# Kernel tuning notes

Measured on AMD Instinct MI355X. Metric: run time of the kernel, lower is better.

The kernel has to match this reference:

```python
import jax, jax.numpy as jnp
import numpy as np

DECAY = 0.999
EPS = 1e-06
NUM_CLUSTERS = 512
NUM_HEADS = 8
DIM_PER_HEAD = 64


def setup_inputs() -> dict:
    key = jax.random.key(0)
    k1, k2 = jax.random.split(key)
    x = jax.random.normal(k1, (8, 2048, NUM_HEADS * DIM_PER_HEAD), dtype=jnp.float32)
    means = jax.random.normal(k2, (NUM_HEADS, NUM_CLUSTERS, DIM_PER_HEAD), dtype=jnp.float32)
    return {"x": x, "means": means}


def reference(x, means):
    b, n, _ = x.shape
    h, k, d = means.shape
    xh = x.reshape(b, n, h, d)  # 'b n (h d) -> b n h d'
    dists = (
        jnp.sum(xh ** 2, axis=-1)[..., None]
        - 2.0 * jnp.einsum('bnhd,hkd->bnhk', xh, means)
        + jnp.sum(means ** 2, axis=-1)[None, None, :, :]
    )
    cluster_ids = jnp.argmin(dists, axis=-1)  # [b, n, h] int
    # training-path EMA codebook update
    one_hot = jax.nn.one_hot(cluster_ids, k, dtype=jnp.float32)  # [b, n, h, k]
    per_cluster_count = jnp.sum(one_hot, axis=(0, 1))  # [h, k]
    sum_x = jnp.einsum('bnhk,bnhd->hkd', one_hot, xh)  # [h, k, d]
    new_means = sum_x / (EPS + per_cluster_count[..., None])
    updated_means = (1.0 - DECAY) * new_means + DECAY * means
    return cluster_ids, updated_means
```

## Files before the change

kernel.cpp:

```cpp
#include <hip/hip_runtime.h>

#define NUM_HEADS 8
#define DIM 64
#define NCLUST 512
#define NTOK 16384
#define ROWLEN 512
#define NIDS (NTOK * NUM_HEADS)
#define NMEANS (NUM_HEADS * NCLUST * DIM)
#define NCK (NUM_HEADS * NCLUST)
#define TPB 64
#define KQ 128
#define CAP 8
#define DELTA 0.35f

typedef unsigned long long u64;
typedef short bf16x8 __attribute__((ext_vector_type(8)));
typedef float f32x4 __attribute__((ext_vector_type(4)));

__device__ __forceinline__ unsigned short f2bf(float f) {
    unsigned b = __float_as_uint(f);
    return (unsigned short)((b + 0x7fffu + ((b >> 16) & 1u)) >> 16);
}
__device__ __forceinline__ unsigned pack2bf(float lo, float hi) {
    return (unsigned)f2bf(lo) | ((unsigned)f2bf(hi) << 16);
}
__device__ __forceinline__ float bf2f(unsigned short b) {
    return __uint_as_float((unsigned)b << 16);
}
__device__ __forceinline__ u64 packkey(float s, int k) {
    unsigned u = __float_as_uint(s);
    unsigned ord = (u & 0x80000000u) ? ~u : (u | 0x80000000u);
    return ((u64)(~ord) << 32) | (unsigned)k;
}
__device__ __forceinline__ int swz(int row, int byte_in_row) {
    return row * 128 + (byte_in_row ^ ((row & 7) << 4));
}

__global__ void vq_prep(const float* __restrict__ means,
                        float* __restrict__ q,
                        unsigned short* __restrict__ mbf) {
    int g = blockIdx.x * blockDim.x + threadIdx.x;
    int row = g >> 4, c = g & 15;
    float4 v = *(const float4*)(means + (size_t)row * DIM + c * 4);
    ushort4 b;
    b.x = f2bf(v.x); b.y = f2bf(v.y); b.z = f2bf(v.z); b.w = f2bf(v.w);
    *(ushort4*)(mbf + (size_t)row * DIM + c * 4) = b;
    float s = fmaf(v.x, v.x, fmaf(v.y, v.y, fmaf(v.z, v.z, v.w * v.w)));
#pragma unroll
    for (int off = 1; off < 16; off <<= 1) s += __shfl_xor(s, off, 64);
    if (c == 0) q[row] = 0.5f * s;
}

__global__ __launch_bounds__(256, 8) void vq_score(const float* __restrict__ x,
                                                   const float* __restrict__ means,
                                                   const unsigned short* __restrict__ mbf,
                                                   const float* __restrict__ q,
                                                   float* __restrict__ ids_f) {
    __shared__ __align__(16) unsigned char msq[KQ * 128];
    __shared__ float qs[NCLUST];
    __shared__ int cnt[TPB];
    __shared__ unsigned short candL[TPB][CAP];

    const int head = blockIdx.y;
    const int t0   = blockIdx.x * TPB;
    const int tid  = threadIdx.x;
    const int wv = tid >> 6, l = tid & 63;
    const int lg = l >> 4, lc = l & 15;
    const int twave = wv * 16;

    auto stage_async = [&](int qt) {
        const unsigned char* gbase = (const unsigned char*)mbf
            + ((size_t)head * NCLUST + (size_t)qt * KQ) * (DIM * 2);
        const int rloc = l >> 3;
        const int srcb = ((l & 7) << 4) ^ (rloc << 4);
#pragma unroll
        for (int i = 0; i < 4; ++i) {
            int chunk = wv * 4 + i;
            const unsigned char* src = gbase + (chunk * 8 + rloc) * 128 + srcb;
            __builtin_amdgcn_global_load_lds(
                (const __attribute__((address_space(1))) unsigned int*)src,
                (__attribute__((address_space(3))) unsigned int*)(msq + chunk * 1024),
                16, 0, 0);
        }
    };

    bf16x8 af[2];
    {
        const float* xrow = x + (size_t)(t0 + twave + lc) * ROWLEN + head * DIM;
#pragma unroll
        for (int ks = 0; ks < 2; ++ks) {
            float av[8];
            *(float4*)&av[0] = *(const float4*)(xrow + ks * 32 + lg * 8);
            *(float4*)&av[4] = *(const float4*)(xrow + ks * 32 + lg * 8 + 4);
#pragma unroll
            for (int j = 0; j < 8; ++j) af[ks][j] = (short)f2bf(av[j]);
        }
    }
    qs[tid] = q[head * NCLUST + tid];
    qs[tid + 256] = q[head * NCLUST + tid + 256];
    if (tid < TPB) cnt[tid] = 0;
    stage_async(0);
    __syncthreads();

    float best[4];
#pragma unroll
    for (int r = 0; r < 4; ++r) best[r] = -3.0e38f;
    float thr[4];

    auto sweep1_q = [&](int qt) {
        const int rbase = 511 - qt * KQ - lc;
#pragma unroll
        for (int ct = 0; ct < KQ / 16; ++ct) {
            bf16x8 b0 = *(const bf16x8*)(msq + swz(ct * 16 + lc, 0 + lg * 16));
            bf16x8 b1 = *(const bf16x8*)(msq + swz(ct * 16 + lc, 64 + lg * 16));
            float qv = qs[qt * KQ + ct * 16 + lc];
            int rk = rbase - ct * 16;
            f32x4 acc = (f32x4){-qv, -qv, -qv, -qv};
            acc = __builtin_amdgcn_mfma_f32_16x16x32_bf16(af[0], b0, acc, 0, 0, 0);
            acc = __builtin_amdgcn_mfma_f32_16x16x32_bf16(af[1], b1, acc, 0, 0, 0);
#pragma unroll
            for (int r = 0; r < 4; ++r) {
                float v = __uint_as_float((__float_as_uint(acc[r]) & 0xFFFFFE00u) | (unsigned)rk);
                best[r] = fmaxf(best[r], v);
            }
        }
    };
    auto collect_q = [&](int qt) {
#pragma unroll
        for (int ct = 0; ct < KQ / 16; ++ct) {
            bf16x8 b0 = *(const bf16x8*)(msq + swz(ct * 16 + lc, 0 + lg * 16));
            bf16x8 b1 = *(const bf16x8*)(msq + swz(ct * 16 + lc, 64 + lg * 16));
            float qv = qs[qt * KQ + ct * 16 + lc];
            int k = qt * KQ + ct * 16 + lc;
            f32x4 acc = (f32x4){-qv, -qv, -qv, -qv};
            acc = __builtin_amdgcn_mfma_f32_16x16x32_bf16(af[0], b0, acc, 0, 0, 0);
            acc = __builtin_amdgcn_mfma_f32_16x16x32_bf16(af[1], b1, acc, 0, 0, 0);
#pragma unroll
            for (int r = 0; r < 4; ++r) {
                if (acc[r] >= thr[r]) {
                    int tok = twave + lg * 4 + r;
                    int slot = atomicAdd(&cnt[tok], 1);
                    if (slot < CAP) candL[tok][slot] = (unsigned short)k;
                }
            }
        }
    };

    for (int qt = 0; qt < 4; ++qt) {
        sweep1_q(qt);
        if (qt < 3) {
            __syncthreads();
            stage_async(qt + 1);
            __syncthreads();
        }
    }
#pragma unroll
    for (int r = 0; r < 4; ++r) {
#pragma unroll
        for (int off = 1; off < 16; off <<= 1)
            best[r] = fmaxf(best[r], __shfl_xor(best[r], off, 64));
        thr[r] = best[r] - DELTA;
    }

    collect_q(3);
    for (int qt = 2; qt >= 0; --qt) {
        __syncthreads();
        stage_async(qt);
        __syncthreads();
        collect_q(qt);
    }
    __syncthreads();

#pragma unroll
    for (int g = 0; g < 4; ++g) {
        int tok = twave + g * 4 + lg;
        int n = cnt[tok]; n = n < CAP ? n : CAP;
        const float4 xv = *(const float4*)(x + (size_t)(t0 + tok) * ROWLEN + head * DIM + lc * 4);
        u64 bk = ~0ull;
        for (int j = 0; j < n; ++j) {
            int k = candL[tok][j];
            const float4 mv = *(const float4*)(means + ((size_t)head * NCLUST + k) * DIM + lc * 4);
            float p = fmaf(xv.x, mv.x, fmaf(xv.y, mv.y, fmaf(xv.z, mv.z, xv.w * mv.w)));
#pragma unroll
            for (int off = 1; off < 16; off <<= 1) p += __shfl_xor(p, off, 64);
            u64 cd = packkey(p - qs[k], k);
            bk = cd < bk ? cd : bk;
        }
        if (lc == 0) ids_f[(size_t)(t0 + tok) * NUM_HEADS + head] = (float)(unsigned)(bk & 0x1ffu);
    }
}

__global__ void vq_scatter(const float* __restrict__ x,
                           const float* __restrict__ ids_f,
                           float* __restrict__ counts,
                           unsigned short* __restrict__ sums_bf,
                           int rep_mask) {
    int g = blockIdx.x * blockDim.x + threadIdx.x;
    int p = g >> 5;
    int l32 = threadIdx.x & 31;
    int token = p >> 3;
    int h = p & 7;
    int rep = token & rep_mask;
    int id = (int)ids_f[p];
    float2 xv = *(const float2*)(x + (size_t)token * ROWLEN + h * DIM + l32 * 2);
    unsigned val = pack2bf(xv.x, xv.y);
    unsigned short* dst = sums_bf + (size_t)rep * NMEANS
                        + (((size_t)h * NCLUST + id) << 6) + l32 * 2;
    asm volatile("global_atomic_pk_add_bf16 %0, %1, off" :: "v"(dst), "v"(val) : "memory");
    if (l32 == 0) atomicAdd(&counts[rep * NCK + h * NCLUST + id], 1.0f);
}

__global__ void vq_final(const float* __restrict__ means,
                         const float* __restrict__ counts,
                         const unsigned short* __restrict__ sums_bf,
                         float* __restrict__ out_means,
                         int nrep) {
    int i = blockIdx.x * blockDim.x + threadIdx.x;
    int ck = i >> 6;
    float c = 0.f, s = 0.f;
    for (int r = 0; r < nrep; ++r) {
        c += counts[r * NCK + ck];
        s += bf2f(sums_bf[(size_t)r * NMEANS + i]);
    }
    float nm = s / (1e-6f + c);
    out_means[i] = 0.999f * means[i] + 0.001f * nm;
}

extern "C" void kernel_launch(void* const* d_in, const int* in_sizes, int n_in,
                              void* d_out, int out_size, void* d_ws, size_t ws_size,
                              hipStream_t stream) {
    const float* x     = (const float*)d_in[0];
    const float* means = (const float*)d_in[1];

    float* out       = (float*)d_out;
    float* ids_f     = out;
    float* out_means = out + NIDS;

    float*          q   = (float*)d_ws;
    unsigned short* mbf = (unsigned short*)(q + NCK);
    float*          fbase = (float*)(mbf + NMEANS);
    size_t core = (size_t)((char*)fbase - (char*)d_ws);

    size_t per_rep = (size_t)NCK * sizeof(float) + (size_t)NMEANS * sizeof(unsigned short);
    int nrep = 1;
    for (int r = 8; r > 1; r >>= 1) {
        if (ws_size >= core + (size_t)r * per_rep) { nrep = r; break; }
    }
    float*          counts  = fbase;
    unsigned short* sums_bf = (unsigned short*)(counts + (size_t)nrep * NCK);

    hipMemsetAsync(counts, 0, (size_t)nrep * per_rep, stream);

    vq_prep<<<(NCK * 16) / 256, 256, 0, stream>>>(means, q, mbf);

    dim3 gs(NTOK / TPB, NUM_HEADS);
    vq_score<<<gs, 256, 0, stream>>>(x, means, mbf, q, ids_f);

    vq_scatter<<<(NIDS * 32) / 256, 256, 0, stream>>>(x, ids_f, counts, sums_bf, nrep - 1);

    vq_final<<<NMEANS / 256, 256, 0, stream>>>(means, counts, sums_bf, out_means, nrep);
}
```

Baseline: 75.52 us.

## Double-buffer codebook tiles and process two token tiles per wave

Each wave now handles 32 tokens (two 16-row A fragments), so every codebook B fragment read from LDS feeds twice as many MFMAs. The LDS staging buffer is doubled so the next quarter of the codebook loads asynchronously while the current one is swept, which removes one barrier per step. The collect pass reuses the last two resident buffers before reloading the first two. The index-packing trick in the max sweep is dropped, leaving a plain fmax. The cost is higher register and LDS use and fewer blocks, with launch bounds lowered from 8 to 4, and the pipelining depends on the asynchronous LDS loads completing before the barrier.

```diff
diff --git a/kernel.cpp b/kernel.cpp
--- a/kernel.cpp
+++ b/kernel.cpp
@@ -8,7 +8,7 @@
 #define NIDS (NTOK * NUM_HEADS)
 #define NMEANS (NUM_HEADS * NCLUST * DIM)
 #define NCK (NUM_HEADS * NCLUST)
-#define TPB 64
+#define TPB 128
 #define KQ 128
 #define CAP 8
 #define DELTA 0.35f
@@ -51,12 +51,12 @@
     if (c == 0) q[row] = 0.5f * s;
 }
 
-__global__ __launch_bounds__(256, 8) void vq_score(const float* __restrict__ x,
+__global__ __launch_bounds__(256, 4) void vq_score(const float* __restrict__ x,
                                                    const float* __restrict__ means,
                                                    const unsigned short* __restrict__ mbf,
                                                    const float* __restrict__ q,
                                                    float* __restrict__ ids_f) {
-    __shared__ __align__(16) unsigned char msq[KQ * 128];
+    __shared__ __align__(16) unsigned char msq[2][KQ * 128];
     __shared__ float qs[NCLUST];
     __shared__ int cnt[TPB];
     __shared__ unsigned short candL[TPB][CAP];
@@ -66,9 +66,9 @@
     const int tid  = threadIdx.x;
     const int wv = tid >> 6, l = tid & 63;
     const int lg = l >> 4, lc = l & 15;
-    const int twave = wv * 16;
-
-    auto stage_async = [&](int qt) {
+    const int twave = wv * 32;
+
+    auto stage_async = [&](int qt, int b) {
         const unsigned char* gbase = (const unsigned char*)mbf
             + ((size_t)head * NCLUST + (size_t)qt * KQ) * (DIM * 2);
         const int rloc = l >> 3;
@@ -79,100 +79,104 @@
             const unsigned char* src = gbase + (chunk * 8 + rloc) * 128 + srcb;
             __builtin_amdgcn_global_load_lds(
                 (const __attribute__((address_space(1))) unsigned int*)src,
-                (__attribute__((address_space(3))) unsigned int*)(msq + chunk * 1024),
+                (__attribute__((address_space(3))) unsigned int*)(&msq[b][0] + chunk * 1024),
                 16, 0, 0);
         }
     };
 
-    bf16x8 af[2];
-    {
-        const float* xrow = x + (size_t)(t0 + twave + lc) * ROWLEN + head * DIM;
+    bf16x8 af[2][2];
+#pragma unroll
+    for (int tt = 0; tt < 2; ++tt) {
+        const float* xrow = x + (size_t)(t0 + twave + tt * 16 + lc) * ROWLEN + head * DIM;
 #pragma unroll
         for (int ks = 0; ks < 2; ++ks) {
             float av[8];
             *(float4*)&av[0] = *(const float4*)(xrow + ks * 32 + lg * 8);
             *(float4*)&av[4] = *(const float4*)(xrow + ks * 32 + lg * 8 + 4);
 #pragma unroll
-            for (int j = 0; j < 8; ++j) af[ks][j] = (short)f2bf(av[j]);
+            for (int j = 0; j < 8; ++j) af[tt][ks][j] = (short)f2bf(av[j]);
         }
     }
     qs[tid] = q[head * NCLUST + tid];
     qs[tid + 256] = q[head * NCLUST + tid + 256];
     if (tid < TPB) cnt[tid] = 0;
-    stage_async(0);
-    __syncthreads();
-
-    float best[4];
-#pragma unroll
-    for (int r = 0; r < 4; ++r) best[r] = -3.0e38f;
-    float thr[4];
-
-    auto sweep1_q = [&](int qt) {
-        const int rbase = 511 - qt * KQ - lc;
+    stage_async(0, 0);
+    __syncthreads();
+
+    float best[2][4];
+#pragma unroll
+    for (int tt = 0; tt < 2; ++tt)
+#pragma unroll
+        for (int r = 0; r < 4; ++r) best[tt][r] = -3.0e38f;
+    float thr[2][4];
+
+    auto sweep1_q = [&](int qt, int b) {
 #pragma unroll
         for (int ct = 0; ct < KQ / 16; ++ct) {
-            bf16x8 b0 = *(const bf16x8*)(msq + swz(ct * 16 + lc, 0 + lg * 16));
-            bf16x8 b1 = *(const bf16x8*)(msq + swz(ct * 16 + lc, 64 + lg * 16));
+            bf16x8 b0 = *(const bf16x8*)(&msq[b][0] + swz(ct * 16 + lc, 0 + lg * 16));
+            bf16x8 b1 = *(const bf16x8*)(&msq[b][0] + swz(ct * 16 + lc, 64 + lg * 16));
             float qv = qs[qt * KQ + ct * 16 + lc];
-            int rk = rbase - ct * 16;
-            f32x4 acc = (f32x4){-qv, -qv, -qv, -qv};
-            acc = __builtin_amdgcn_mfma_f32_16x16x32_bf16(af[0], b0, acc, 0, 0, 0);
-            acc = __builtin_amdgcn_mfma_f32_16x16x32_bf16(af[1], b1, acc, 0, 0, 0);
-#pragma unroll
-            for (int r = 0; r < 4; ++r) {
-                float v = __uint_as_float((__float_as_uint(acc[r]) & 0xFFFFFE00u) | (unsigned)rk);
-                best[r] = fmaxf(best[r], v);
+#pragma unroll
+            for (int tt = 0; tt < 2; ++tt) {
+                f32x4 acc = (f32x4){-qv, -qv, -qv, -qv};
+                acc = __builtin_amdgcn_mfma_f32_16x16x32_bf16(af[tt][0], b0, acc, 0, 0, 0);
+                acc = __builtin_amdgcn_mfma_f32_16x16x32_bf16(af[tt][1], b1, acc, 0, 0, 0);
+#pragma unroll
+                for (int r = 0; r < 4; ++r)
+                    best[tt][r] = fmaxf(best[tt][r], acc[r]);
             }
         }
     };
-    auto collect_q = [&](int qt) {
+    auto collect_q = [&](int qt, int b) {
 #pragma unroll
         for (int ct = 0; ct < KQ / 16; ++ct) {
-            bf16x8 b0 = *(const bf16x8*)(msq + swz(ct * 16 + lc, 0 + lg * 16));
-            bf16x8 b1 = *(const bf16x8*)(msq + swz(ct * 16 + lc, 64 + lg * 16));
+            bf16x8 b0 = *(const bf16x8*)(&msq[b][0] + swz(ct * 16 + lc, 0 + lg * 16));
+            bf16x8 b1 = *(const bf16x8*)(&msq[b][0] + swz(ct * 16 + lc, 64 + lg * 16));
             float qv = qs[qt * KQ + ct * 16 + lc];
             int k = qt * KQ + ct * 16 + lc;
-            f32x4 acc = (f32x4){-qv, -qv, -qv, -qv};
-            acc = __builtin_amdgcn_mfma_f32_16x16x32_bf16(af[0], b0, acc, 0, 0, 0);
-            acc = __builtin_amdgcn_mfma_f32_16x16x32_bf16(af[1], b1, acc, 0, 0, 0);
-#pragma unroll
-            for (int r = 0; r < 4; ++r) {
-                if (acc[r] >= thr[r]) {
-                    int tok = twave + lg * 4 + r;
-                    int slot = atomicAdd(&cnt[tok], 1);
-                    if (slot < CAP) candL[tok][slot] = (unsigned short)k;
+#pragma unroll
+            for (int tt = 0; tt < 2; ++tt) {
+                f32x4 acc = (f32x4){-qv, -qv, -qv, -qv};
+                acc = __builtin_amdgcn_mfma_f32_16x16x32_bf16(af[tt][0], b0, acc, 0, 0, 0);
+                acc = __builtin_amdgcn_mfma_f32_16x16x32_bf16(af[tt][1], b1, acc, 0, 0, 0);
+#pragma unroll
+                for (int r = 0; r < 4; ++r) {
+                    if (acc[r] >= thr[tt][r]) {
+                        int tok = twave + tt * 16 + lg * 4 + r;
+                        int slot = atomicAdd(&cnt[tok], 1);
+                        if (slot < CAP) candL[tok][slot] = (unsigned short)k;
+                    }
                 }
             }
         }
     };
 
     for (int qt = 0; qt < 4; ++qt) {
-        sweep1_q(qt);
-        if (qt < 3) {
-            __syncthreads();
-            stage_async(qt + 1);
-            __syncthreads();
-        }
-    }
-#pragma unroll
-    for (int r = 0; r < 4; ++r) {
-#pragma unroll
-        for (int off = 1; off < 16; off <<= 1)
-            best[r] = fmaxf(best[r], __shfl_xor(best[r], off, 64));
-        thr[r] = best[r] - DELTA;
-    }
-
-    collect_q(3);
-    for (int qt = 2; qt >= 0; --qt) {
-        __syncthreads();
-        stage_async(qt);
-        __syncthreads();
-        collect_q(qt);
-    }
-    __syncthreads();
-
-#pragma unroll
-    for (int g = 0; g < 4; ++g) {
+        if (qt < 3) stage_async(qt + 1, (qt + 1) & 1);
+        sweep1_q(qt, qt & 1);
+        if (qt < 3) __syncthreads();
+    }
+#pragma unroll
+    for (int tt = 0; tt < 2; ++tt)
+#pragma unroll
+        for (int r = 0; r < 4; ++r) {
+#pragma unroll
+            for (int off = 1; off < 16; off <<= 1)
+                best[tt][r] = fmaxf(best[tt][r], __shfl_xor(best[tt][r], off, 64));
+            thr[tt][r] = best[tt][r] - DELTA;
+        }
+
+    collect_q(3, 1);
+    collect_q(2, 0);
+    __syncthreads();
+    stage_async(1, 1);
+    stage_async(0, 0);
+    __syncthreads();
+    collect_q(1, 1);
+    collect_q(0, 0);
+    __syncthreads();
+
+    for (int g = 0; g < 8; ++g) {
         int tok = twave + g * 4 + lg;
         int n = cnt[tok]; n = n < CAP ? n : CAP;
         const float4 xv = *(const float4*)(x + (size_t)(t0 + tok) * ROWLEN + head * DIM + lc * 4);
```

Result: no change. 75.67 us (+0.2%).

## Fuse max sweep and candidate collection into a single pass with running threshold

Applied to the files above, without the earlier changes.

Replaces the two-pass scheme (full sweep to find the max score, then restaging all four codebook quarters to collect candidates) with a single pass. Each quarter's scores are kept in registers, and candidates are gathered against a running threshold. This halves MFMA work and codebook staging, at the cost of more candidates from looser early thresholds. CAP is raised to 16, overflowing tokens fall back to a full exact scan over all 512 clusters, and launch bounds drop to 4 blocks per SM to make room for the extra registers.

```diff
diff --git a/kernel.cpp b/kernel.cpp
--- a/kernel.cpp
+++ b/kernel.cpp
@@ -10,7 +10,7 @@
 #define NCK (NUM_HEADS * NCLUST)
 #define TPB 64
 #define KQ 128
-#define CAP 8
+#define CAP 16
 #define DELTA 0.35f
 
 typedef unsigned long long u64;
@@ -51,7 +51,7 @@
     if (c == 0) q[row] = 0.5f * s;
 }
 
-__global__ __launch_bounds__(256, 8) void vq_score(const float* __restrict__ x,
+__global__ __launch_bounds__(256, 4) void vq_score(const float* __restrict__ x,
                                                    const float* __restrict__ means,
                                                    const unsigned short* __restrict__ mbf,
                                                    const float* __restrict__ q,
@@ -105,86 +105,74 @@
     float best[4];
 #pragma unroll
     for (int r = 0; r < 4; ++r) best[r] = -3.0e38f;
-    float thr[4];
-
-    auto sweep1_q = [&](int qt) {
-        const int rbase = 511 - qt * KQ - lc;
-#pragma unroll
-        for (int ct = 0; ct < KQ / 16; ++ct) {
+
+    for (int qt = 0; qt < 4; ++qt) {
+        f32x4 A[8];
+#pragma unroll
+        for (int ct = 0; ct < 8; ++ct) {
             bf16x8 b0 = *(const bf16x8*)(msq + swz(ct * 16 + lc, 0 + lg * 16));
             bf16x8 b1 = *(const bf16x8*)(msq + swz(ct * 16 + lc, 64 + lg * 16));
             float qv = qs[qt * KQ + ct * 16 + lc];
-            int rk = rbase - ct * 16;
             f32x4 acc = (f32x4){-qv, -qv, -qv, -qv};
             acc = __builtin_amdgcn_mfma_f32_16x16x32_bf16(af[0], b0, acc, 0, 0, 0);
             acc = __builtin_amdgcn_mfma_f32_16x16x32_bf16(af[1], b1, acc, 0, 0, 0);
+            A[ct] = acc;
+        }
+        __syncthreads();
+        if (qt < 3) stage_async(qt + 1);
+
+#pragma unroll
+        for (int ct = 0; ct < 8; ++ct)
+#pragma unroll
+            for (int r = 0; r < 4; ++r) best[r] = fmaxf(best[r], A[ct][r]);
+        float thr[4];
+#pragma unroll
+        for (int r = 0; r < 4; ++r) {
+#pragma unroll
+            for (int off = 1; off < 16; off <<= 1)
+                best[r] = fmaxf(best[r], __shfl_xor(best[r], off, 64));
+            thr[r] = best[r] - DELTA;
+        }
+#pragma unroll
+        for (int ct = 0; ct < 8; ++ct) {
+            int k = qt * KQ + ct * 16 + lc;
 #pragma unroll
             for (int r = 0; r < 4; ++r) {
-                float v = __uint_as_float((__float_as_uint(acc[r]) & 0xFFFFFE00u) | (unsigned)rk);
-                best[r] = fmaxf(best[r], v);
-            }
-        }
-    };
-    auto collect_q = [&](int qt) {
-#pragma unroll
-        for (int ct = 0; ct < KQ / 16; ++ct) {
-            bf16x8 b0 = *(const bf16x8*)(msq + swz(ct * 16 + lc, 0 + lg * 16));
-            bf16x8 b1 = *(const bf16x8*)(msq + swz(ct * 16 + lc, 64 + lg * 16));
-            float qv = qs[qt * KQ + ct * 16 + lc];
-            int k = qt * KQ + ct * 16 + lc;
-            f32x4 acc = (f32x4){-qv, -qv, -qv, -qv};
-            acc = __builtin_amdgcn_mfma_f32_16x16x32_bf16(af[0], b0, acc, 0, 0, 0);
-            acc = __builtin_amdgcn_mfma_f32_16x16x32_bf16(af[1], b1, acc, 0, 0, 0);
-#pragma unroll
-            for (int r = 0; r < 4; ++r) {
-                if (acc[r] >= thr[r]) {
+                if (A[ct][r] >= thr[r]) {
                     int tok = twave + lg * 4 + r;
                     int slot = atomicAdd(&cnt[tok], 1);
                     if (slot < CAP) candL[tok][slot] = (unsigned short)k;
                 }
             }
         }
-    };
-
-    for (int qt = 0; qt < 4; ++qt) {
-        sweep1_q(qt);
-        if (qt < 3) {
-            __syncthreads();
-            stage_async(qt + 1);
-            __syncthreads();
-        }
-    }
-#pragma unroll
-    for (int r = 0; r < 4; ++r) {
-#pragma unroll
-        for (int off = 1; off < 16; off <<= 1)
-            best[r] = fmaxf(best[r], __shfl_xor(best[r], off, 64));
-        thr[r] = best[r] - DELTA;
-    }
-
-    collect_q(3);
-    for (int qt = 2; qt >= 0; --qt) {
         __syncthreads();
-        stage_async(qt);
-        __syncthreads();
-        collect_q(qt);
-    }
-    __syncthreads();
+    }
 
 #pragma unroll
     for (int g = 0; g < 4; ++g) {
         int tok = twave + g * 4 + lg;
-        int n = cnt[tok]; n = n < CAP ? n : CAP;
+        int n = cnt[tok];
         const float4 xv = *(const float4*)(x + (size_t)(t0 + tok) * ROWLEN + head * DIM + lc * 4);
         u64 bk = ~0ull;
-        for (int j = 0; j < n; ++j) {
-            int k = candL[tok][j];
-            const float4 mv = *(const float4*)(means + ((size_t)head * NCLUST + k) * DIM + lc * 4);
-            float p = fmaf(xv.x, mv.x, fmaf(xv.y, mv.y, fmaf(xv.z, mv.z, xv.w * mv.w)));
-#pragma unroll
-            for (int off = 1; off < 16; off <<= 1) p += __shfl_xor(p, off, 64);
-            u64 cd = packkey(p - qs[k], k);
-            bk = cd < bk ? cd : bk;
+        if (n > CAP) {
+            for (int k = 0; k < NCLUST; ++k) {
+                const float4 mv = *(const float4*)(means + ((size_t)head * NCLUST + k) * DIM + lc * 4);
+                float p = fmaf(xv.x, mv.x, fmaf(xv.y, mv.y, fmaf(xv.z, mv.z, xv.w * mv.w)));
+#pragma unroll
+                for (int off = 1; off < 16; off <<= 1) p += __shfl_xor(p, off, 64);
+                u64 cd = packkey(p - qs[k], k);
+                bk = cd < bk ? cd : bk;
+            }
+        } else {
+            for (int j = 0; j < n; ++j) {
+                int k = candL[tok][j];
+                const float4 mv = *(const float4*)(means + ((size_t)head * NCLUST + k) * DIM + lc * 4);
+                float p = fmaf(xv.x, mv.x, fmaf(xv.y, mv.y, fmaf(xv.z, mv.z, xv.w * mv.w)));
+#pragma unroll
+                for (int off = 1; off < 16; off <<= 1) p += __shfl_xor(p, off, 64);
+                u64 cd = packkey(p - qs[k], k);
+                bk = cd < bk ? cd : bk;
+            }
         }
         if (lc == 0) ids_f[(size_t)(t0 + tok) * NUM_HEADS + head] = (float)(unsigned)(bk & 0x1ffu);
     }
```

Result: slower. 84.70 us (+12.2%).
